# Optimization experiments

Hardware: AMD Instinct MI355X
Metric: run time of the kernel (lower is better)

## Reference

```python
import jax, jax.numpy as jnp
import numpy as np
import jax.lax as lax

H, D, C, CS, NS, OW, PD = 8, 64, 512, 64, 5, 8, 1
MAX_LR = 0.1
KCONV = 4


def short_conv(x, w, b):
    # x: (B,T,Din) -> causal depthwise conv over time
    B, T, Din = x.shape
    xc = jnp.transpose(x, (0, 2, 1))
    xc = jnp.pad(xc, ((0, 0), (0, 0), (KCONV - 1, 0)))
    xc = lax.conv_general_dilated(xc, w, window_strides=(1,), padding='VALID',
                                  dimension_numbers=('NCW', 'OIW', 'NCW'),
                                  feature_group_count=Din)
    xc = xc + b[:, jnp.newaxis]
    return jnp.transpose(xc, (0, 2, 1))


def linear_scan(h_init, gates, inputs):
    # h_t = gate_t * h_{t-1} + input_t ; gates: (B,cs,H), inputs: (B,cs,H,...)
    extra = inputs.ndim - gates.ndim
    g = gates.reshape(gates.shape + (1,) * extra)
    first = g[:, 0:1] * h_init[:, jnp.newaxis] + inputs[:, 0:1]
    mod_in = jnp.concatenate([first, inputs[:, 1:]], axis=1)
    mod_g = jnp.concatenate([jnp.zeros_like(g[:, 0:1]), g[:, 1:]], axis=1)

    def assoc(a, bb):
        ga, xa = a
        gb, xb = bb
        return (ga * gb, gb * xa + xb)

    _, h_all = lax.associative_scan(assoc, (mod_g, mod_in), axis=1)
    return h_all, h_all[:, -1]


def omega_aggregate(u, gamma, w):
    cs = u.shape[1]
    cum = jnp.cumsum(gamma * u, axis=1)
    if w >= cs:
        return cum
    shifted = jnp.concatenate([jnp.zeros_like(cum[:, :w]), cum[:, :-w]], axis=1)
    return cum - shifted


def polar_express(S, steps):
    # Newton-Schulz quintic orthogonalization (Muon/Polar-Express coefficients)
    a, b, c = 3.4445, -4.7750, 2.0315
    n = jnp.sqrt(jnp.sum(S * S, axis=(-2, -1), keepdims=True))
    X = S / (n * 1.01 + 1e-7)
    for _ in range(steps):
        A = X @ jnp.swapaxes(X, -2, -1)
        X = a * X + (b * A + c * (A @ A)) @ X
    return X


def rms_norm(x):
    ms = jnp.mean(x * x, axis=-1, keepdims=True)
    return x * lax.rsqrt(ms + 1e-6)


def atlas_forward(x, Wq, Wk, Wv, Wproj, conv_q_w, conv_q_b, conv_k_w, conv_k_b,
                  conv_v_w, conv_v_b, ga_w, ga_b, ge_w, ge_b, gt_w, gt_b,
                  gg_w, gg_b, poly_coeffs, ln_gamma, W1_init, rg_w):
    B, T, _ = x.shape
    q = short_conv(x @ Wq.T, conv_q_w, conv_q_b).reshape(B, T, H, D)
    k = short_conv(x @ Wk.T, conv_k_w, conv_k_b).reshape(B, T, H, D)
    v = short_conv(x @ Wv.T, conv_v_w, conv_v_b).reshape(B, T, H, D)

    def phi(z):
        r = poly_coeffs[0] * z
        zp = z
        for i in range(1, PD):
            zp = zp * z
            r = r + poly_coeffs[i] * zp
        return r

    q, k = phi(q), phi(k)

    alpha = jax.nn.sigmoid(x @ ga_w.T + ga_b)          # (B,T,H) memory retention
    eta = MAX_LR * jax.nn.sigmoid(x @ ge_w.T + ge_b)   # learning rate
    theta = jax.nn.sigmoid(x @ gt_w.T + gt_b)          # momentum decay
    gamma = jax.nn.sigmoid(x @ gg_w.T + gg_b)          # omega context gate

    nC = T // CS

    def chunk(z):
        return jnp.moveaxis(z.reshape(B, nC, CS, *z.shape[2:]), 1, 0)

    q_ch, k_ch, v_ch = chunk(q), chunk(k), chunk(v)
    a_ch = chunk(alpha)[..., None]
    e_ch = chunk(eta)[..., None]
    t_ch = chunk(theta)[..., None]
    g_ch = chunk(gamma)[..., None]

    M0 = jnp.broadcast_to(W1_init, (B, H, D, D))
    S0 = jnp.zeros((B, H, D, D), x.dtype)

    def step(carry, inp):
        M, S = carry
        q_c, k_c, v_c, a_c, e_c, t_c, g_c = inp
        pred = jnp.einsum('bhvk,bchk->bchv', M, k_c)
        err = pred - v_c
        u = (2.0 / D) * jnp.einsum('bchv,bchk->bchvk', err, k_c)
        u = omega_aggregate(u, g_c[..., None], OW)
        mom_in = -(e_c[..., None] * u)
        chunk_S, S = linear_scan(S, jnp.squeeze(t_c, -1), mom_in)
        chunk_S_orth = polar_express(chunk_S, NS)
        M_all, M = linear_scan(M, jnp.squeeze(a_c, -1), chunk_S_orth)
        y_c = jnp.einsum('bchvk,bchk->bchv', M_all, q_c)
        return (M, S), y_c

    (_, _), y = lax.scan(step, (M0, S0), (q_ch, k_ch, v_ch, a_ch, e_ch, t_ch, g_ch))
    y = jnp.moveaxis(y, 0, 1).reshape(B, T, H, D)
    y = rms_norm(y) * (1.0 + ln_gamma)
    rg = jax.nn.sigmoid(x @ rg_w.T)          # (B,T,H) retrieve gate
    y = y * rg[..., None]
    return y.reshape(B, T, H * D) @ Wproj.T


def setup_inputs() -> dict:
    key = jax.random.key(0)
    ks = jax.random.split(key, 24)
    B, T = 2, 1024
    Din = H * D

    def lin(k, o, i):
        return jax.random.normal(k, (o, i), jnp.float32) * (1.0 / np.sqrt(i))

    bound = float(np.sqrt(6.0 / (D + D)))
    return dict(
        x=jax.random.normal(ks[0], (B, T, C), jnp.float32),
        Wq=lin(ks[1], Din, C), Wk=lin(ks[2], Din, C), Wv=lin(ks[3], Din, C),
        Wproj=lin(ks[4], C, Din),
        conv_q_w=jax.random.normal(ks[5], (Din, 1, KCONV), jnp.float32) * 0.02,
        conv_q_b=jnp.zeros(Din, jnp.float32),
        conv_k_w=jax.random.normal(ks[6], (Din, 1, KCONV), jnp.float32) * 0.02,
        conv_k_b=jnp.zeros(Din, jnp.float32),
        conv_v_w=jax.random.normal(ks[7], (Din, 1, KCONV), jnp.float32) * 0.02,
        conv_v_b=jnp.zeros(Din, jnp.float32),
        ga_w=lin(ks[8], H, C), ga_b=jnp.zeros(H, jnp.float32),
        ge_w=lin(ks[9], H, C), ge_b=jnp.zeros(H, jnp.float32),
        gt_w=lin(ks[10], H, C), gt_b=jnp.zeros(H, jnp.float32),
        gg_w=lin(ks[11], H, C), gg_b=jnp.zeros(H, jnp.float32),
        poly_coeffs=jnp.ones(PD, jnp.float32),
        ln_gamma=jnp.zeros((H, D), jnp.float32),
        W1_init=jax.random.uniform(ks[12], (H, D, D), jnp.float32, -bound, bound),
        rg_w=lin(ks[13], H, C),
    )


def reference(x, Wq, Wk, Wv, Wproj, conv_q_w, conv_q_b, conv_k_w, conv_k_b,
              conv_v_w, conv_v_b, ga_w, ga_b, ge_w, ge_b, gt_w, gt_b,
              gg_w, gg_b, poly_coeffs, ln_gamma, W1_init, rg_w):
    return atlas_forward(x, Wq, Wk, Wv, Wproj, conv_q_w, conv_q_b, conv_k_w,
                         conv_k_b, conv_v_w, conv_v_b, ga_w, ga_b, ge_w, ge_b,
                         gt_w, gt_b, gg_w, gg_b, poly_coeffs, ln_gamma,
                         W1_init, rg_w)
```

## Files before the change

kernel.cpp:

```cpp
#include <hip/hip_runtime.h>

#define B_ 2
#define T_ 1024
#define H_ 8
#define D_ 64
#define SW(r, c) ((c) ^ (((r) & 7) << 3))

typedef __attribute__((ext_vector_type(8))) short s8v;
typedef __attribute__((ext_vector_type(4))) short s4v;
typedef __attribute__((ext_vector_type(4))) float f4v;

__device__ __forceinline__ short f2bf(float f) {
  unsigned u = __float_as_uint(f);
  u += 0x7fffu + ((u >> 16) & 1u);
  return (short)(u >> 16);
}
__device__ __forceinline__ float bf2f(short s) {
  return __uint_as_float(((unsigned)(unsigned short)s) << 16);
}
__device__ __forceinline__ float sigm(float v) { return 1.0f / (1.0f + __expf(-v)); }

#define MFMA(a, b, c) __builtin_amdgcn_mfma_f32_16x16x32_bf16((a), (b), (c), 0, 0, 0)

__global__ __launch_bounds__(256) void gemm_bt(const float* __restrict__ A,
// ... 73 lines not shown
}

__global__ __launch_bounds__(256) void gemm_qkv(const float* __restrict__ A,
    const float* __restrict__ Wq, const float* __restrict__ Wk,
    const float* __restrict__ Wv,
    float* __restrict__ xq, float* __restrict__ xk, float* __restrict__ xv) {
  __shared__ short Ash[64][40], Asl[64][40];
  __shared__ short Bsh[64][40], Bsl[64][40];
  const int sel = blockIdx.y >> 3;
  const float* Bw = sel == 0 ? Wq : (sel == 1 ? Wk : Wv);
  float* Co = sel == 0 ? xq : (sel == 1 ? xk : xv);
  const int tid = threadIdx.x;
  const int lane = tid & 63;
  const int wv = tid >> 6;
  const int wr = (wv >> 1) * 32;
  const int wc = (wv & 1) * 32;
  const int m0 = blockIdx.x * 64;
  const int n0 = (blockIdx.y & 7) * 64;
  const int ldr = tid >> 2;
  const int ldc = (tid & 3) * 8;
  const int l15 = lane & 15;
  const int kq = (lane >> 4) * 8;
  f4v acc[2][2];
#pragma unroll
  for (int i = 0; i < 2; ++i)
#pragma unroll
    for (int j = 0; j < 2; ++j)
#pragma unroll
      for (int r = 0; r < 4; ++r) acc[i][j][r] = 0.0f;
  const float* ap = A + (size_t)(m0 + ldr) * 512 + ldc;
  const float* bp = Bw + (size_t)(n0 + ldr) * 512 + ldc;
#pragma unroll 1
  for (int kt = 0; kt < 512; kt += 32) {
    float4 av0 = *(const float4*)(ap + kt);
    float4 av1 = *(const float4*)(ap + kt + 4);
    float4 bv0 = *(const float4*)(bp + kt);
    float4 bv1 = *(const float4*)(bp + kt + 4);
    float af[8] = {av0.x, av0.y, av0.z, av0.w, av1.x, av1.y, av1.z, av1.w};
    float bf[8] = {bv0.x, bv0.y, bv0.z, bv0.w, bv1.x, bv1.y, bv1.z, bv1.w};
    s8v ah, al, bh, bl;
#pragma unroll
    for (int i = 0; i < 8; ++i) {
      short h = f2bf(af[i]); ah[i] = h; al[i] = f2bf(af[i] - bf2f(h));
      h = f2bf(bf[i]); bh[i] = h; bl[i] = f2bf(bf[i] - bf2f(h));
    }
    __syncthreads();
    *(s8v*)&Ash[ldr][ldc] = ah; *(s8v*)&Asl[ldr][ldc] = al;
    *(s8v*)&Bsh[ldr][ldc] = bh; *(s8v*)&Bsl[ldr][ldc] = bl;
    __syncthreads();
    s8v a0h = *(const s8v*)&Ash[wr + l15][kq];
    s8v a1h = *(const s8v*)&Ash[wr + 16 + l15][kq];
    s8v b0h = *(const s8v*)&Bsh[wc + l15][kq];
    s8v b1h = *(const s8v*)&Bsh[wc + 16 + l15][kq];
    s8v a0l = *(const s8v*)&Asl[wr + l15][kq];
    s8v a1l = *(const s8v*)&Asl[wr + 16 + l15][kq];
    s8v b0l = *(const s8v*)&Bsl[wc + l15][kq];
    s8v b1l = *(const s8v*)&Bsl[wc + 16 + l15][kq];
    acc[0][0] = MFMA(a0h, b0h, acc[0][0]);
    acc[0][1] = MFMA(a0h, b1h, acc[0][1]);
    acc[1][0] = MFMA(a1h, b0h, acc[1][0]);
    acc[1][1] = MFMA(a1h, b1h, acc[1][1]);
    acc[0][0] = MFMA(a0h, b0l, acc[0][0]);
    acc[0][1] = MFMA(a0h, b1l, acc[0][1]);
    acc[1][0] = MFMA(a1h, b0l, acc[1][0]);
    acc[1][1] = MFMA(a1h, b1l, acc[1][1]);
    acc[0][0] = MFMA(a0l, b0h, acc[0][0]);
    acc[0][1] = MFMA(a0l, b1h, acc[0][1]);
    acc[1][0] = MFMA(a1l, b0h, acc[1][0]);
    acc[1][1] = MFMA(a1l, b1h, acc[1][1]);
  }
#pragma unroll
  for (int m2 = 0; m2 < 2; ++m2)
#pragma unroll
    for (int n2 = 0; n2 < 2; ++n2)
#pragma unroll
      for (int r = 0; r < 4; ++r) {
        int row = m0 + wr + m2 * 16 + (lane >> 4) * 4 + r;
        int col = n0 + wc + n2 * 16 + l15;
        Co[(size_t)row * 512 + col] = acc[m2][n2][r];
      }
}

__global__ __launch_bounds__(256) void conv3_k(
    const float* __restrict__ xq, const float* __restrict__ xk,
    const float* __restrict__ xv,
    const float* __restrict__ cqw, const float* __restrict__ cqb,
    const float* __restrict__ ckw, const float* __restrict__ ckb,
    const float* __restrict__ cvw, const float* __restrict__ cvb,
    const float* __restrict__ pc,
    float* __restrict__ qb, float* __restrict__ kb, float* __restrict__ vb) {
  const int s = blockIdx.x >> 12;
  const int idx = ((blockIdx.x & 4095) << 8) + threadIdx.x;
  const float* in = s == 0 ? xq : (s == 1 ? xk : xv);
  const float* w  = s == 0 ? cqw : (s == 1 ? ckw : cvw);
  const float* bs = s == 0 ? cqb : (s == 1 ? ckb : cvb);
  float* o        = s == 0 ? qb : (s == 1 ? kb : vb);
  const int d = idx & 511;
  const int bt = idx >> 9;
  const int t = bt & (T_ - 1);
  float acc = bs[d];
#pragma unroll
  for (int j = 0; j < 4; ++j) {
    int tt = t - 3 + j;
    if (tt >= 0) acc += w[d * 4 + j] * in[(size_t)(bt - 3 + j) * 512 + d];
  }
  float sc = (s < 2) ? pc[0] : 1.0f;
  o[idx] = sc * acc;
}

__global__ __launch_bounds__(256) void gates_k(const float* __restrict__ x,
    const float* __restrict__ gaw, const float* __restrict__ gab,
    const float* __restrict__ gew, const float* __restrict__ geb,
    const float* __restrict__ gtw, const float* __restrict__ gtb,
    const float* __restrict__ ggw, const float* __restrict__ ggb,
    const float* __restrict__ rgw,
    float* __restrict__ alpha, float* __restrict__ eta,
    float* __restrict__ theta, float* __restrict__ gam, float* __restrict__ rg) {
  int wv = threadIdx.x >> 6, lane = threadIdx.x & 63;
  int bt = blockIdx.x * 4 + wv;
  float xr[8];
#pragma unroll
  for (int i = 0; i < 8; ++i) xr[i] = x[(size_t)bt * 512 + i * 64 + lane];
  for (int h = 0; h < 8; ++h) {
    float s0 = 0, s1 = 0, s2 = 0, s3 = 0, s4 = 0;
#pragma unroll
    for (int i = 0; i < 8; ++i) {
      float xv = xr[i];
      int o = h * 512 + i * 64 + lane;
      s0 += xv * gaw[o];
      s1 += xv * gew[o];
      s2 += xv * gtw[o];
      s3 += xv * ggw[o];
      s4 += xv * rgw[o];
    }
#pragma unroll
    for (int off = 32; off >= 1; off >>= 1) {
      s0 += __shfl_xor(s0, off);
      s1 += __shfl_xor(s1, off);
      s2 += __shfl_xor(s2, off);
      s3 += __shfl_xor(s3, off);
      s4 += __shfl_xor(s4, off);
    }
    if (lane == 0) {
      size_t o = (size_t)bt * 8 + h;
      alpha[o] = sigm(s0 + gab[h]);
      eta[o]   = 0.1f * sigm(s1 + geb[h]);
      theta[o] = sigm(s2 + gtb[h]);
      gam[o]   = sigm(s3 + ggb[h]);
      rg[o]    = sigm(s4);
    }
  }
}

__global__ __launch_bounds__(256) void init_carry(const float* __restrict__ w1,
    float* __restrict__ Mc, float* __restrict__ Sc) {
  int idx = blockIdx.x * 256 + threadIdx.x;
  Mc[idx] = w1[idx & 32767];
  Sc[idx] = 0.0f;
}

__global__ __launch_bounds__(256) void chunk_a(
    const float* __restrict__ kb, const float* __restrict__ vb,
    const float* __restrict__ eta, const float* __restrict__ theta,
    const float* __restrict__ gam,
    const float* __restrict__ Mc, float* __restrict__ Sc,
    float* __restrict__ chS, int ci) {
  __shared__ float KT[64][65];
  __shared__ float errl[4][68];
  __shared__ float Ml[4][64];
  __shared__ float ge_[64], gt_[64], gg_[64];
  const int tid = threadIdx.x;
  const int bh = blockIdx.x >> 4;
  const int vs = blockIdx.x & 15;
  const int b = bh >> 3, h = bh & 7;
  const int v0 = vs * 4;
  const int t0 = ci * 64;
  const int lane = tid & 63, q4 = tid >> 6;
  for (int it = 0; it < 16; ++it) {
    int c = it * 4 + q4;
    KT[lane][c] = kb[((size_t)(b * T_ + t0 + c) * H_ + h) * 64 + lane];
  }
  if (tid < 64) {
    size_t gi = (size_t)(b * T_ + t0 + tid) * H_ + h;
    ge_[tid] = eta[gi]; gt_[tid] = theta[gi]; gg_[tid] = gam[gi];
  }
  Ml[q4][lane] = Mc[((size_t)bh * 64 + v0 + q4) * 64 + lane];
  __syncthreads();
  {
    int c = lane, vr = q4;
    float p = 0.0f;
#pragma unroll
    for (int k2 = 0; k2 < 64; ++k2) p += KT[k2][c] * Ml[vr][k2];
    float vv = vb[((size_t)(b * T_ + t0 + c) * H_ + h) * 64 + v0 + vr];
    errl[vr][c] = p - vv;
  }
  __syncthreads();
  {
    const int kk = lane, vr = q4, v = v0 + vr;
    float S = Sc[((size_t)bh * 64 + v) * 64 + kk];
    float ring[8];
    float cum = 0.0f;
    float* out = chS + ((size_t)(b << 6) * 8 + h) * 4096 + (size_t)v * 64 + kk;
    for (int c8 = 0; c8 < 8; ++c8) {
#pragma unroll
      for (int j = 0; j < 8; ++j) {
        int c = c8 * 8 + j;
        float u = 0.03125f * errl[vr][c] * KT[kk][c];
        float gu = gg_[c] * u;
        cum += gu;
        if (c8 > 0) cum -= ring[j];
        ring[j] = gu;
        float mom = -ge_[c] * cum;
        S = gt_[c] * S + mom;
        out[(size_t)c * 32768] = S;
      }
    }
    Sc[((size_t)bh * 64 + v) * 64 + kk] = S;
  }
}

__device__ __forceinline__ void mm4(const short (*Ah)[64], const short (*Al)[64],
    const short (*Bh)[64], const short (*Bl)[64],
    int wr, int wc, int l15, int kq, int sp, f4v acc[2][2]) {
#pragma unroll
  for (int kt = 0; kt < 64; kt += 32) {
    const int ra0 = wr + l15, ra1 = wr + 16 + l15;
    const int rb0 = wc + l15, rb1 = wc + 16 + l15;
    s8v a0h = *(const s8v*)&Ah[ra0][SW(ra0, kt + kq)];
    s8v a1h = *(const s8v*)&Ah[ra1][SW(ra1, kt + kq)];
    s8v b0h = *(const s8v*)&Bh[rb0][SW(rb0, kt + kq)];
    s8v b1h = *(const s8v*)&Bh[rb1][SW(rb1, kt + kq)];
    acc[0][0] = MFMA(a0h, b0h, acc[0][0]);
    acc[0][1] = MFMA(a0h, b1h, acc[0][1]);
    acc[1][0] = MFMA(a1h, b0h, acc[1][0]);
    acc[1][1] = MFMA(a1h, b1h, acc[1][1]);
    if (sp) {
      s8v a0l = *(const s8v*)&Al[ra0][SW(ra0, kt + kq)];
      s8v a1l = *(const s8v*)&Al[ra1][SW(ra1, kt + kq)];
      s8v b0l = *(const s8v*)&Bl[rb0][SW(rb0, kt + kq)];
      s8v b1l = *(const s8v*)&Bl[rb1][SW(rb1, kt + kq)];
      acc[0][0] = MFMA(a0h, b0l, acc[0][0]);
      acc[0][1] = MFMA(a0h, b1l, acc[0][1]);
      acc[1][0] = MFMA(a1h, b0l, acc[1][0]);
      acc[1][1] = MFMA(a1h, b1l, acc[1][1]);
      acc[0][0] = MFMA(a0l, b0h, acc[0][0]);
      acc[0][1] = MFMA(a0l, b1h, acc[0][1]);
      acc[1][0] = MFMA(a1l, b0h, acc[1][0]);
      acc[1][1] = MFMA(a1l, b1h, acc[1][1]);
    }
  }
}

__global__ __launch_bounds__(256, 3) void polar_k(float* __restrict__ cs) {
  __shared__ short Xh[64][64], Xl[64][64];
  __shared__ short XTh[64][64], XTl[64][64];
  __shared__ short Zh[64][64], Zl[64][64];
  __shared__ float red[4];
  const int tid = threadIdx.x;
  const int lane = tid & 63;
  const int w = tid >> 6;
  const int wr = (w >> 1) * 32;
  const int wc = (w & 1) * 32;
  const int l15 = lane & 15;
  const int q4 = lane >> 4;
  const int kq = q4 * 8;
  float* base = cs + (size_t)blockIdx.x * 4096;
  float xr[2][2][4];
  float ss = 0.0f;
#pragma unroll
  for (int m2 = 0; m2 < 2; ++m2)
#pragma unroll
    for (int n2 = 0; n2 < 2; ++n2)
#pragma unroll
      for (int r = 0; r < 4; ++r) {
        float v = base[(wr + m2 * 16 + q4 * 4 + r) * 64 + wc + n2 * 16 + l15];
        xr[m2][n2][r] = v;
        ss += v * v;
      }
#pragma unroll
  for (int off = 32; off >= 1; off >>= 1) ss += __shfl_xor(ss, off);
  if (lane == 0) red[w] = ss;
  __syncthreads();
  float scale = 1.0f / (sqrtf(red[0] + red[1] + red[2] + red[3]) * 1.01f + 1e-7f);
#pragma unroll
  for (int m2 = 0; m2 < 2; ++m2)
#pragma unroll
    for (int n2 = 0; n2 < 2; ++n2) {
      const int rr0 = wr + m2 * 16 + q4 * 4;
      const int cc = wc + n2 * 16 + l15;
      s4v hv, lv;
#pragma unroll
      for (int r = 0; r < 4; ++r) {
        float xv = xr[m2][n2][r] * scale;
        xr[m2][n2][r] = xv;
        short hh = f2bf(xv);
        short ll = f2bf(xv - bf2f(hh));
        hv[r] = hh; lv[r] = ll;
        Xh[rr0 + r][SW(rr0 + r, cc)] = hh;
        Xl[rr0 + r][SW(rr0 + r, cc)] = ll;
      }
      *(s4v*)&XTh[cc][SW(cc, rr0)] = hv;
      *(s4v*)&XTl[cc][SW(cc, rr0)] = lv;
    }
  __syncthreads();

#pragma unroll 1
  for (int it = 0; it < 5; ++it) {
    const int sp = (it < 4);
    f4v at[2][2];
#pragma unroll
    for (int m2 = 0; m2 < 2; ++m2)
#pragma unroll
      for (int n2 = 0; n2 < 2; ++n2)
#pragma unroll
        for (int r = 0; r < 4; ++r) at[m2][n2][r] = 0.0f;
    mm4(XTh, XTl, XTh, XTl, wr, wc, l15, kq, sp, at);
#pragma unroll
    for (int m2 = 0; m2 < 2; ++m2)
#pragma unroll
      for (int n2 = 0; n2 < 2; ++n2) {
        const int rr0 = wr + m2 * 16 + q4 * 4;
        const int cc = wc + n2 * 16 + l15;
        s4v hv, lv;
#pragma unroll
        for (int r = 0; r < 4; ++r) {
          float a = at[m2][n2][r];
          short hh = f2bf(a);
          hv[r] = hh; lv[r] = f2bf(a - bf2f(hh));
        }
        *(s4v*)&Zh[cc][SW(cc, rr0)] = hv;
        if (sp) *(s4v*)&Zl[cc][SW(cc, rr0)] = lv;
      }
    __syncthreads();
    f4v a2[2][2];
#pragma unroll
    for (int m2 = 0; m2 < 2; ++m2)
#pragma unroll
      for (int n2 = 0; n2 < 2; ++n2)
#pragma unroll
        for (int r = 0; r < 4; ++r) a2[m2][n2][r] = 0.0f;
    mm4(Zh, Zl, Zh, Zl, wr, wc, l15, kq, sp, a2);
    float zt[2][2][4];
#pragma unroll
    for (int m2 = 0; m2 < 2; ++m2)
#pragma unroll
      for (int n2 = 0; n2 < 2; ++n2)
#pragma unroll
        for (int r = 0; r < 4; ++r)
          zt[m2][n2][r] = -4.7750f * at[m2][n2][r] + 2.0315f * a2[m2][n2][r];
    __syncthreads();
#pragma unroll
    for (int m2 = 0; m2 < 2; ++m2)
#pragma unroll
      for (int n2 = 0; n2 < 2; ++n2) {
        const int rr0 = wr + m2 * 16 + q4 * 4;
        const int cc = wc + n2 * 16 + l15;
        s4v hv, lv;
#pragma unroll
        for (int r = 0; r < 4; ++r) {
          float zv = zt[m2][n2][r];
          short hh = f2bf(zv);
          hv[r] = hh; lv[r] = f2bf(zv - bf2f(hh));
        }
        *(s4v*)&Zh[cc][SW(cc, rr0)] = hv;
        if (sp) *(s4v*)&Zl[cc][SW(cc, rr0)] = lv;
      }
    __syncthreads();
    f4v q3[2][2];
#pragma unroll
    for (int m2 = 0; m2 < 2; ++m2)
#pragma unroll
      for (int n2 = 0; n2 < 2; ++n2)
#pragma unroll
        for (int r = 0; r < 4; ++r) q3[m2][n2][r] = 0.0f;
    mm4(Xh, Xl, Zh, Zl, wr, wc, l15, kq, sp, q3);
#pragma unroll
    for (int m2 = 0; m2 < 2; ++m2)
#pragma unroll
      for (int n2 = 0; n2 < 2; ++n2)
#pragma unroll
        for (int r = 0; r < 4; ++r)
          xr[m2][n2][r] = 3.4445f * xr[m2][n2][r] + q3[m2][n2][r];
    if (it < 4) {
      __syncthreads();
      const int slo = (it < 3);
#pragma unroll
      for (int m2 = 0; m2 < 2; ++m2)
#pragma unroll
        for (int n2 = 0; n2 < 2; ++n2) {
          const int rr0 = wr + m2 * 16 + q4 * 4;
          const int cc = wc + n2 * 16 + l15;
          s4v hv, lv;
#pragma unroll
          for (int r = 0; r < 4; ++r) {
            float xv = xr[m2][n2][r];
            short hh = f2bf(xv);
            short ll = f2bf(xv - bf2f(hh));
            hv[r] = hh; lv[r] = ll;
            Xh[rr0 + r][SW(rr0 + r, cc)] = hh;
            if (slo) Xl[rr0 + r][SW(rr0 + r, cc)] = ll;
          }
          *(s4v*)&XTh[cc][SW(cc, rr0)] = hv;
          if (slo) *(s4v*)&XTl[cc][SW(cc, rr0)] = lv;
        }
      __syncthreads();
    }
  }
#pragma unroll
  for (int m2 = 0; m2 < 2; ++m2)
#pragma unroll
    for (int n2 = 0; n2 < 2; ++n2)
#pragma unroll
      for (int r = 0; r < 4; ++r)
        base[(wr + m2 * 16 + q4 * 4 + r) * 64 + wc + n2 * 16 + l15] = xr[m2][n2][r];
}

__global__ __launch_bounds__(256, 1) void chunk_ca(
    const float* __restrict__ qb, const float* __restrict__ kb,
    const float* __restrict__ vb,
    const float* __restrict__ alpha, const float* __restrict__ eta,
    const float* __restrict__ theta, const float* __restrict__ gam,
    float* __restrict__ Mc, float* __restrict__ Sc,
    float* __restrict__ chS, float* __restrict__ yb, int ci) {
  __shared__ float KT[64][65];
  __shared__ float errl[4][68];
  __shared__ float Ml[4][64];
  __shared__ float ge_[64], gt_[64], gg_[64];
  const int tid = threadIdx.x, lane = tid & 63, w = tid >> 6;
  const int bh = blockIdx.x >> 4, vs = blockIdx.x & 15;
  const int b = bh >> 3, h = bh & 7;
  const int v0 = vs * 4, v = v0 + w;
  const int t0 = ci * 64;
  float M = Mc[((size_t)bh * 64 + v) * 64 + lane];
  const float* op = chS + ((size_t)(b << 6) * 8 + h) * 4096 + (size_t)v * 64 + lane;
  const float* qp = qb + ((size_t)(b * T_ + t0) * 8 + h) * 64 + lane;
  float* yp = yb + ((size_t)(b * T_ + t0) * 8 + h) * 64 + v;
  float av = alpha[(size_t)(b * T_ + t0 + lane) * 8 + h];
#pragma unroll
  for (int half = 0; half < 2; ++half) {
    const int cb = half * 32;
    float ov[32], qv[32], p[32];
#pragma unroll
    for (int j = 0; j < 32; ++j) ov[j] = op[(size_t)(cb + j) * 32768];
#pragma unroll
    for (int j = 0; j < 32; ++j) qv[j] = qp[(size_t)(cb + j) * 512];
#pragma unroll
    for (int j = 0; j < 32; ++j) {
      M = __builtin_fmaf(__shfl(av, cb + j), M, ov[j]);
      p[j] = M * qv[j];
    }
#pragma unroll
    for (int j = 0; j < 32; ++j) {
#pragma unroll
      for (int off = 32; off >= 1; off >>= 1) p[j] += __shfl_xor(p[j], off);
    }
    if (lane == 0) {
#pragma unroll
      for (int j = 0; j < 32; ++j) yp[(size_t)(cb + j) * 512] = p[j];
    }
  }
  Mc[((size_t)bh * 64 + v) * 64 + lane] = M;
  if (ci == 15) return;
  const int t1 = t0 + 64;
  Ml[w][lane] = M;
  for (int it = 0; it < 16; ++it) {
    int c = it * 4 + w;
    KT[lane][c] = kb[((size_t)(b * T_ + t1 + c) * 8 + h) * 64 + lane];
  }
  if (tid < 64) {
    size_t gi = (size_t)(b * T_ + t1 + tid) * 8 + h;
    ge_[tid] = eta[gi]; gt_[tid] = theta[gi]; gg_[tid] = gam[gi];
  }
  __syncthreads();
  {
    int c = lane, vr = w;
    float s0 = 0, s1 = 0, s2 = 0, s3 = 0;
#pragma unroll
    for (int k2 = 0; k2 < 64; k2 += 4) {
      s0 += KT[k2 + 0][c] * Ml[vr][k2 + 0];
      s1 += KT[k2 + 1][c] * Ml[vr][k2 + 1];
      s2 += KT[k2 + 2][c] * Ml[vr][k2 + 2];
      s3 += KT[k2 + 3][c] * Ml[vr][k2 + 3];
    }
    float vv = vb[((size_t)(b * T_ + t1 + c) * 8 + h) * 64 + v0 + vr];
    errl[vr][c] = (s0 + s1) + (s2 + s3) - vv;
  }
  __syncthreads();
  {
    const int kk = lane, vr = w, vv2 = v0 + vr;
    float S = Sc[((size_t)bh * 64 + vv2) * 64 + kk];
    float ring[8];
    float cum = 0.0f;
    float* out = chS + ((size_t)(b << 6) * 8 + h) * 4096 + (size_t)vv2 * 64 + kk;
    for (int c8 = 0; c8 < 8; ++c8) {
#pragma unroll
      for (int j = 0; j < 8; ++j) {
        int c = c8 * 8 + j;
        float u = 0.03125f * errl[vr][c] * KT[kk][c];
        float gu = gg_[c] * u;
        cum += gu;
        if (c8 > 0) cum -= ring[j];
        ring[j] = gu;
        float mom = -ge_[c] * cum;
        S = gt_[c] * S + mom;
        out[(size_t)c * 32768] = S;
      }
    }
    Sc[((size_t)bh * 64 + vv2) * 64 + kk] = S;
  }
}

__global__ __launch_bounds__(256) void norm_k(const float* __restrict__ yb,
    const float* __restrict__ lng, const float* __restrict__ rg,
    float* __restrict__ yn) {
  const int lane = threadIdx.x & 63;
  const int gw = blockIdx.x * 4 + (threadIdx.x >> 6);
  const int h = gw & 7;
  const int bt = gw >> 3;
  float y = yb[(size_t)gw * 64 + lane];
  float s = y * y;
#pragma unroll
  for (int off = 32; off >= 1; off >>= 1) s += __shfl_xor(s, off);
  float r = rsqrtf(s * (1.0f / 64.0f) + 1e-6f);
  yn[(size_t)gw * 64 + lane] = y * r * (1.0f + lng[h * 64 + lane]) * rg[(size_t)bt * 8 + h];
}

extern "C" void kernel_launch(void* const* d_in, const int* in_sizes, int n_in,
                              void* d_out, int out_size, void* d_ws, size_t ws_size,
                              hipStream_t stream) {
  (void)in_sizes; (void)n_in; (void)out_size; (void)ws_size;
  const float* x   = (const float*)d_in[0];
  const float* Wq  = (const float*)d_in[1];
  const float* Wk  = (const float*)d_in[2];
  const float* Wv  = (const float*)d_in[3];
  const float* Wpr = (const float*)d_in[4];
  const float* cqw = (const float*)d_in[5];
  const float* cqb = (const float*)d_in[6];
  const float* ckw = (const float*)d_in[7];
  const float* ckb = (const float*)d_in[8];
  const float* cvw = (const float*)d_in[9];
  const float* cvb = (const float*)d_in[10];
  const float* gaw = (const float*)d_in[11];
  const float* gab = (const float*)d_in[12];
  const float* gew = (const float*)d_in[13];
  const float* geb = (const float*)d_in[14];
  const float* gtw = (const float*)d_in[15];
  const float* gtb = (const float*)d_in[16];
  const float* ggw = (const float*)d_in[17];
  const float* ggb = (const float*)d_in[18];
  const float* pc  = (const float*)d_in[19];
  const float* lng = (const float*)d_in[20];
  const float* w1  = (const float*)d_in[21];
  const float* rgw = (const float*)d_in[22];
  float* outp = (float*)d_out;

  float* chS = (float*)d_ws;
  float* xq = chS;
  float* xk = chS + 1048576;
  float* xv = chS + 2 * 1048576;
  float* yn = chS;
  char* wp = (char*)d_ws + (size_t)16 * 1024 * 1024;
  auto alloc = [&](size_t bytes) {
    char* p = wp;
    wp += (bytes + 255) & ~(size_t)255;
    return p;
  };
  const size_t BT = (size_t)B_ * T_;
  float* qb = (float*)alloc(BT * 512 * 4);
  float* kb = (float*)alloc(BT * 512 * 4);
  float* vb = (float*)alloc(BT * 512 * 4);
  float* yb = (float*)alloc(BT * 512 * 4);
  float* alpha = (float*)alloc(BT * 8 * 4);
  float* eta   = (float*)alloc(BT * 8 * 4);
  float* theta = (float*)alloc(BT * 8 * 4);
  float* gam   = (float*)alloc(BT * 8 * 4);
  float* rg    = (float*)alloc(BT * 8 * 4);
  float* Mc = (float*)alloc((size_t)65536 * 4);
  float* Sc = (float*)alloc((size_t)65536 * 4);

  init_carry<<<dim3(256), dim3(256), 0, stream>>>(w1, Mc, Sc);
  gemm_qkv<<<dim3(32, 24), dim3(256), 0, stream>>>(x, Wq, Wk, Wv, xq, xk, xv);
  conv3_k<<<dim3(12288), dim3(256), 0, stream>>>(xq, xk, xv, cqw, cqb, ckw, ckb,
                                                 cvw, cvb, pc, qb, kb, vb);
  gates_k<<<dim3(512), dim3(256), 0, stream>>>(x, gaw, gab, gew, geb, gtw, gtb,
                                               ggw, ggb, rgw, alpha, eta, theta, gam, rg);
  chunk_a<<<dim3(256), dim3(256), 0, stream>>>(kb, vb, eta, theta, gam, Mc, Sc, chS, 0);
  for (int ci = 0; ci < 16; ++ci) {
    polar_k<<<dim3(1024), dim3(256), 0, stream>>>(chS);
    chunk_ca<<<dim3(256), dim3(256), 0, stream>>>(qb, kb, vb, alpha, eta, theta, gam,
                                                  Mc, Sc, chS, yb, ci);
  }
  norm_k<<<dim3(4096), dim3(256), 0, stream>>>(yb, lng, rg, yn);
  gemm_bt<<<dim3(32, 8), dim3(256), 0, stream>>>(yn, Wpr, outp, 2048, 512, 512);
}
```

Baseline: 1.048 ms.

## Fuse chunk recurrence and polar iterations into one persistent kernel with flag barriers

Replaces the 33 per-chunk launches of chunk_a/polar_k/chunk_ca with a single persistent kernel of 512 blocks. The blocks for each batch-head pair synchronise through global atomic counters instead of kernel boundaries, and the M/S carries stay in registers instead of going through global memory. Warps 2-3 prefetch the next chunk's keys and gates while warps 0-1 run the output phase. This removes launch and drain overhead, at the cost of spin-wait barriers that require all 512 blocks to be co-resident, plus lower parallelism per phase.

```diff
diff --git a/kernel.cpp b/kernel.cpp
--- a/kernel.cpp
+++ b/kernel.cpp
@@ -249,169 +249,178 @@
   }
 }
 
-__global__ __launch_bounds__(256) void init_carry(const float* __restrict__ w1,
-    float* __restrict__ Mc, float* __restrict__ Sc) {
-  int idx = blockIdx.x * 256 + threadIdx.x;
-  Mc[idx] = w1[idx & 32767];
-  Sc[idx] = 0.0f;
-}
-
-__global__ __launch_bounds__(256) void chunk_a(
-    const float* __restrict__ kb, const float* __restrict__ vb,
+__global__ __launch_bounds__(256, 2) void atlas_persist(
+    const float* __restrict__ qb, const float* __restrict__ kb,
+    const float* __restrict__ vb, const float* __restrict__ alpha,
     const float* __restrict__ eta, const float* __restrict__ theta,
-    const float* __restrict__ gam,
-    const float* __restrict__ Mc, float* __restrict__ Sc,
-    float* __restrict__ chS, int ci) {
-  __shared__ float KT[64][65];
-  __shared__ float errl[4][68];
-  __shared__ float Ml[4][64];
-  __shared__ float ge_[64], gt_[64], gg_[64];
-  const int tid = threadIdx.x;
-  const int bh = blockIdx.x >> 4;
-  const int vs = blockIdx.x & 15;
-  const int b = bh >> 3, h = bh & 7;
-  const int v0 = vs * 4;
-  const int t0 = ci * 64;
-  const int lane = tid & 63, q4 = tid >> 6;
-  for (int it = 0; it < 16; ++it) {
-    int c = it * 4 + q4;
-    KT[lane][c] = kb[((size_t)(b * T_ + t0 + c) * H_ + h) * 64 + lane];
-  }
-  if (tid < 64) {
-    size_t gi = (size_t)(b * T_ + t0 + tid) * H_ + h;
-    ge_[tid] = eta[gi]; gt_[tid] = theta[gi]; gg_[tid] = gam[gi];
-  }
-  Ml[q4][lane] = Mc[((size_t)bh * 64 + v0 + q4) * 64 + lane];
-  __syncthreads();
-  {
-    int c = lane, vr = q4;
-    float p = 0.0f;
-#pragma unroll
-    for (int k2 = 0; k2 < 64; ++k2) p += KT[k2][c] * Ml[vr][k2];
-    float vv = vb[((size_t)(b * T_ + t0 + c) * H_ + h) * 64 + v0 + vr];
-    errl[vr][c] = p - vv;
-  }
-  __syncthreads();
-  {
-    const int kk = lane, vr = q4, v = v0 + vr;
-    float S = Sc[((size_t)bh * 64 + v) * 64 + kk];
-    float ring[8];
-    float cum = 0.0f;
-    float* out = chS + ((size_t)(b << 6) * 8 + h) * 4096 + (size_t)v * 64 + kk;
-    for (int c8 = 0; c8 < 8; ++c8) {
-#pragma unroll
-      for (int j = 0; j < 8; ++j) {
-        int c = c8 * 8 + j;
-        float u = 0.03125f * errl[vr][c] * KT[kk][c];
-        float gu = gg_[c] * u;
-        cum += gu;
-        if (c8 > 0) cum -= ring[j];
-        ring[j] = gu;
-        float mom = -ge_[c] * cum;
-        S = gt_[c] * S + mom;
-        out[(size_t)c * 32768] = S;
-      }
-    }
-    Sc[((size_t)bh * 64 + v) * 64 + kk] = S;
-  }
-}
-
-__device__ __forceinline__ void mm4(const short (*Ah)[64], const short (*Al)[64],
-    const short (*Bh)[64], const short (*Bl)[64],
-    int wr, int wc, int l15, int kq, int sp, f4v acc[2][2]) {
-#pragma unroll
-  for (int kt = 0; kt < 64; kt += 32) {
-    const int ra0 = wr + l15, ra1 = wr + 16 + l15;
-    const int rb0 = wc + l15, rb1 = wc + 16 + l15;
-    s8v a0h = *(const s8v*)&Ah[ra0][SW(ra0, kt + kq)];
-    s8v a1h = *(const s8v*)&Ah[ra1][SW(ra1, kt + kq)];
-    s8v b0h = *(const s8v*)&Bh[rb0][SW(rb0, kt + kq)];
-    s8v b1h = *(const s8v*)&Bh[rb1][SW(rb1, kt + kq)];
-    acc[0][0] = MFMA(a0h, b0h, acc[0][0]);
-    acc[0][1] = MFMA(a0h, b1h, acc[0][1]);
-    acc[1][0] = MFMA(a1h, b0h, acc[1][0]);
-    acc[1][1] = MFMA(a1h, b1h, acc[1][1]);
-    if (sp) {
-      s8v a0l = *(const s8v*)&Al[ra0][SW(ra0, kt + kq)];
-      s8v a1l = *(const s8v*)&Al[ra1][SW(ra1, kt + kq)];
-      s8v b0l = *(const s8v*)&Bl[rb0][SW(rb0, kt + kq)];
-      s8v b1l = *(const s8v*)&Bl[rb1][SW(rb1, kt + kq)];
-      acc[0][0] = MFMA(a0h, b0l, acc[0][0]);
-      acc[0][1] = MFMA(a0h, b1l, acc[0][1]);
-      acc[1][0] = MFMA(a1h, b0l, acc[1][0]);
-      acc[1][1] = MFMA(a1h, b1l, acc[1][1]);
-      acc[0][0] = MFMA(a0l, b0h, acc[0][0]);
-      acc[0][1] = MFMA(a0l, b1h, acc[0][1]);
-      acc[1][0] = MFMA(a1l, b0h, acc[1][0]);
-      acc[1][1] = MFMA(a1l, b1h, acc[1][1]);
-    }
-  }
-}
-
-__global__ __launch_bounds__(256, 3) void polar_k(float* __restrict__ cs) {
+    const float* __restrict__ gam, const float* __restrict__ w1,
+    float* __restrict__ chS, float* __restrict__ yb,
+    unsigned* __restrict__ flags) {
   __shared__ short Xh[64][64], Xl[64][64];
   __shared__ short XTh[64][64], XTl[64][64];
   __shared__ short Zh[64][64], Zl[64][64];
   __shared__ float red[4];
+  __shared__ float KT[64][65];
+  __shared__ float Ml[2][64], errl[2][64];
+  __shared__ float ge_[64], gt_[64], gg_[64];
+
   const int tid = threadIdx.x;
   const int lane = tid & 63;
   const int w = tid >> 6;
-  const int wr = (w >> 1) * 32;
-  const int wc = (w & 1) * 32;
-  const int l15 = lane & 15;
-  const int q4 = lane >> 4;
-  const int kq = q4 * 8;
-  float* base = cs + (size_t)blockIdx.x * 4096;
-  float xr[2][2][4];
-  float ss = 0.0f;
-#pragma unroll
-  for (int m2 = 0; m2 < 2; ++m2)
-#pragma unroll
-    for (int n2 = 0; n2 < 2; ++n2)
-#pragma unroll
-      for (int r = 0; r < 4; ++r) {
-        float v = base[(wr + m2 * 16 + q4 * 4 + r) * 64 + wc + n2 * 16 + l15];
-        xr[m2][n2][r] = v;
-        ss += v * v;
-      }
-#pragma unroll
-  for (int off = 32; off >= 1; off >>= 1) ss += __shfl_xor(ss, off);
-  if (lane == 0) red[w] = ss;
-  __syncthreads();
-  float scale = 1.0f / (sqrtf(red[0] + red[1] + red[2] + red[3]) * 1.01f + 1e-7f);
-#pragma unroll
-  for (int m2 = 0; m2 < 2; ++m2)
-#pragma unroll
-    for (int n2 = 0; n2 < 2; ++n2) {
-      const int rr0 = wr + m2 * 16 + q4 * 4;
-      const int cc = wc + n2 * 16 + l15;
-      s4v hv, lv;
-#pragma unroll
-      for (int r = 0; r < 4; ++r) {
-        float xv = xr[m2][n2][r] * scale;
-        xr[m2][n2][r] = xv;
-        short hh = f2bf(xv);
-        short ll = f2bf(xv - bf2f(hh));
-        hv[r] = hh; lv[r] = ll;
-        Xh[rr0 + r][SW(rr0 + r, cc)] = hh;
-        Xl[rr0 + r][SW(rr0 + r, cc)] = ll;
-      }
-      *(s4v*)&XTh[cc][SW(cc, rr0)] = hv;
-      *(s4v*)&XTl[cc][SW(cc, rr0)] = lv;
-    }
-  __syncthreads();
-
-#pragma unroll 1
-  for (int it = 0; it < 5; ++it) {
-    const int sp = (it < 4);
-    f4v at[2][2];
+  const int g = blockIdx.x;
+  const int bh = g & 15, sub = g >> 4;
+  const int b = bh >> 3, h = bh & 7;
+  unsigned* flag = flags + bh * 32;
+  const int wr = (w >> 1) * 32, wc = (w & 1) * 32;
+  const int l15 = lane & 15, q4 = lane >> 4, kq = q4 * 8;
+  const size_t matbase = ((size_t)(b << 6) * 8 + h) * 4096;
+  const int v = 2 * sub + w;
+
+  float M = 0.0f, S = 0.0f;
+
+  auto ARRIVE = [&]() {
+    __threadfence();
+    __syncthreads();
+    if (tid == 0)
+      __hip_atomic_fetch_add(flag, 1u, __ATOMIC_RELEASE, __HIP_MEMORY_SCOPE_AGENT);
+  };
+  auto WAIT = [&](int n) {
+    if (tid == 0) {
+      unsigned tgt = 32u * (unsigned)n;
+      while (__hip_atomic_load(flag, __ATOMIC_ACQUIRE, __HIP_MEMORY_SCOPE_AGENT) < tgt)
+        __builtin_amdgcn_s_sleep(2);
+      __threadfence();
+    }
+    __syncthreads();
+  };
+  auto LOADKT = [&](int cb) {
+    const int t = cb * 64;
+    const int tl = tid - 128;
+    for (int i = tl; i < 4096; i += 128) {
+      int k = i & 63, c = i >> 6;
+      KT[k][c] = kb[((size_t)(b * T_ + t + c) * 8 + h) * 64 + k];
+    }
+    if (tl < 64) {
+      size_t gi = (size_t)(b * T_ + t + tl) * 8 + h;
+      ge_[tl] = eta[gi]; gt_[tl] = theta[gi]; gg_[tl] = gam[gi];
+    }
+  };
+  auto PHASEB = [&](int cb) {
+    const int t = cb * 64;
+    Ml[w][lane] = M;
+    {
+      int c = lane;
+      float s0 = 0, s1 = 0, s2 = 0, s3 = 0;
+#pragma unroll
+      for (int k2 = 0; k2 < 64; k2 += 4) {
+        s0 += KT[k2 + 0][c] * Ml[w][k2 + 0];
+        s1 += KT[k2 + 1][c] * Ml[w][k2 + 1];
+        s2 += KT[k2 + 2][c] * Ml[w][k2 + 2];
+        s3 += KT[k2 + 3][c] * Ml[w][k2 + 3];
+      }
+      float vv = vb[((size_t)(b * T_ + t + c) * 8 + h) * 64 + v];
+      errl[w][c] = (s0 + s1) + (s2 + s3) - vv;
+    }
+    {
+      float ring[8];
+      float cum = 0.0f;
+      float* out = chS + matbase + (size_t)v * 64 + lane;
+      for (int c8 = 0; c8 < 8; ++c8) {
+#pragma unroll
+        for (int j = 0; j < 8; ++j) {
+          int c = c8 * 8 + j;
+          float u = 0.03125f * errl[w][c] * KT[lane][c];
+          float gu = gg_[c] * u;
+          cum += gu;
+          if (c8 > 0) cum -= ring[j];
+          ring[j] = gu;
+          float mom = -ge_[c] * cum;
+          S = gt_[c] * S + mom;
+          out[(size_t)c * 32768] = S;
+        }
+      }
+    }
+  };
+  auto PHASEA = [&](int ci) {
+    const int t0 = ci * 64;
+    const float* op = chS + matbase + (size_t)v * 64 + lane;
+    const float* qp = qb + ((size_t)(b * T_ + t0) * 8 + h) * 64 + lane;
+    float* yp = yb + ((size_t)(b * T_ + t0) * 8 + h) * 64 + v;
+    float av = alpha[(size_t)(b * T_ + t0 + lane) * 8 + h];
+#pragma unroll
+    for (int half = 0; half < 2; ++half) {
+      const int cb2 = half * 32;
+      float ov[32], qv[32], p[32];
+#pragma unroll
+      for (int j = 0; j < 32; ++j) ov[j] = op[(size_t)(cb2 + j) * 32768];
+#pragma unroll
+      for (int j = 0; j < 32; ++j) qv[j] = qp[(size_t)(cb2 + j) * 512];
+#pragma unroll
+      for (int j = 0; j < 32; ++j) {
+        M = __builtin_fmaf(__shfl(av, cb2 + j), M, ov[j]);
+        p[j] = M * qv[j];
+      }
+#pragma unroll
+      for (int j = 0; j < 32; ++j) {
+#pragma unroll
+        for (int off = 32; off >= 1; off >>= 1) p[j] += __shfl_xor(p[j], off);
+      }
+      if (lane == 0) {
+#pragma unroll
+        for (int j = 0; j < 32; ++j) yp[(size_t)(cb2 + j) * 512] = p[j];
+      }
+    }
+  };
+  auto MM4 = [&](const short (*Ah)[64], const short (*Al)[64],
+                 const short (*Bh)[64], const short (*Bl)[64],
+                 int sp, f4v acc[2][2]) {
+#pragma unroll
+    for (int kt = 0; kt < 64; kt += 32) {
+      const int ra0 = wr + l15, ra1 = wr + 16 + l15;
+      const int rb0 = wc + l15, rb1 = wc + 16 + l15;
+      s8v a0h = *(const s8v*)&Ah[ra0][SW(ra0, kt + kq)];
+      s8v a1h = *(const s8v*)&Ah[ra1][SW(ra1, kt + kq)];
+      s8v b0h = *(const s8v*)&Bh[rb0][SW(rb0, kt + kq)];
+      s8v b1h = *(const s8v*)&Bh[rb1][SW(rb1, kt + kq)];
+      acc[0][0] = MFMA(a0h, b0h, acc[0][0]);
+      acc[0][1] = MFMA(a0h, b1h, acc[0][1]);
+      acc[1][0] = MFMA(a1h, b0h, acc[1][0]);
+      acc[1][1] = MFMA(a1h, b1h, acc[1][1]);
+      if (sp) {
+        s8v a0l = *(const s8v*)&Al[ra0][SW(ra0, kt + kq)];
+        s8v a1l = *(const s8v*)&Al[ra1][SW(ra1, kt + kq)];
+        s8v b0l = *(const s8v*)&Bl[rb0][SW(rb0, kt + kq)];
+        s8v b1l = *(const s8v*)&Bl[rb1][SW(rb1, kt + kq)];
+        acc[0][0] = MFMA(a0h, b0l, acc[0][0]);
+        acc[0][1] = MFMA(a0h, b1l, acc[0][1]);
+        acc[1][0] = MFMA(a1h, b0l, acc[1][0]);
+        acc[1][1] = MFMA(a1h, b1l, acc[1][1]);
+        acc[0][0] = MFMA(a0l, b0h, acc[0][0]);
+        acc[0][1] = MFMA(a0l, b1h, acc[0][1]);
+        acc[1][0] = MFMA(a1l, b0h, acc[1][0]);
+        acc[1][1] = MFMA(a1l, b1h, acc[1][1]);
+      }
+    }
+  };
+  auto POLAR = [&](int c) {
+    float* base = chS + ((size_t)((b * 64 + c) * 8) + h) * 4096;
+    float xr[2][2][4];
+    float ss = 0.0f;
 #pragma unroll
     for (int m2 = 0; m2 < 2; ++m2)
 #pragma unroll
       for (int n2 = 0; n2 < 2; ++n2)
 #pragma unroll
-        for (int r = 0; r < 4; ++r) at[m2][n2][r] = 0.0f;
-    mm4(XTh, XTl, XTh, XTl, wr, wc, l15, kq, sp, at);
+        for (int r = 0; r < 4; ++r) {
+          float vv = base[(wr + m2 * 16 + q4 * 4 + r) * 64 + wc + n2 * 16 + l15];
+          xr[m2][n2][r] = vv;
+          ss += vv * vv;
+        }
+#pragma unroll
+    for (int off = 32; off >= 1; off >>= 1) ss += __shfl_xor(ss, off);
+    if (lane == 0) red[w] = ss;
+    __syncthreads();
+    float scale = 1.0f / (sqrtf(red[0] + red[1] + red[2] + red[3]) * 1.01f + 1e-7f);
 #pragma unroll
     for (int m2 = 0; m2 < 2; ++m2)
 #pragma unroll
@@ -421,66 +430,29 @@
         s4v hv, lv;
 #pragma unroll
         for (int r = 0; r < 4; ++r) {
-          float a = at[m2][n2][r];
-          short hh = f2bf(a);
-          hv[r] = hh; lv[r] = f2bf(a - bf2f(hh));
+          float xv = xr[m2][n2][r] * scale;
+          xr[m2][n2][r] = xv;
+          short hh = f2bf(xv);
+          short ll = f2bf(xv - bf2f(hh));
+          hv[r] = hh; lv[r] = ll;
+          Xh[rr0 + r][SW(rr0 + r, cc)] = hh;
+          Xl[rr0 + r][SW(rr0 + r, cc)] = ll;
         }
-        *(s4v*)&Zh[cc][SW(cc, rr0)] = hv;
-        if (sp) *(s4v*)&Zl[cc][SW(cc, rr0)] = lv;
-      }
-    __syncthreads();
-    f4v a2[2][2];
-#pragma unroll
-    for (int m2 = 0; m2 < 2; ++m2)
-#pragma unroll
-      for (int n2 = 0; n2 < 2; ++n2)
-#pragma unroll
-        for (int r = 0; r < 4; ++r) a2[m2][n2][r] = 0.0f;
-    mm4(Zh, Zl, Zh, Zl, wr, wc, l15, kq, sp, a2);
-    float zt[2][2][4];
-#pragma unroll
-    for (int m2 = 0; m2 < 2; ++m2)
-#pragma unroll
-      for (int n2 = 0; n2 < 2; ++n2)
-#pragma unroll
-        for (int r = 0; r < 4; ++r)
-          zt[m2][n2][r] = -4.7750f * at[m2][n2][r] + 2.0315f * a2[m2][n2][r];
-    __syncthreads();
-#pragma unroll
-    for (int m2 = 0; m2 < 2; ++m2)
-#pragma unroll
-      for (int n2 = 0; n2 < 2; ++n2) {
-        const int rr0 = wr + m2 * 16 + q4 * 4;
-        const int cc = wc + n2 * 16 + l15;
-        s4v hv, lv;
-#pragma unroll
-        for (int r = 0; r < 4; ++r) {
-          float zv = zt[m2][n2][r];
-          short hh = f2bf(zv);
-          hv[r] = hh; lv[r] = f2bf(zv - bf2f(hh));
-        }
-        *(s4v*)&Zh[cc][SW(cc, rr0)] = hv;
-        if (sp) *(s4v*)&Zl[cc][SW(cc, rr0)] = lv;
-      }
-    __syncthreads();
-    f4v q3[2][2];
-#pragma unroll
-    for (int m2 = 0; m2 < 2; ++m2)
-#pragma unroll
-      for (int n2 = 0; n2 < 2; ++n2)
-#pragma unroll
-        for (int r = 0; r < 4; ++r) q3[m2][n2][r] = 0.0f;
-    mm4(Xh, Xl, Zh, Zl, wr, wc, l15, kq, sp, q3);
-#pragma unroll
-    for (int m2 = 0; m2 < 2; ++m2)
-#pragma unroll
-      for (int n2 = 0; n2 < 2; ++n2)
-#pragma unroll
-        for (int r = 0; r < 4; ++r)
-          xr[m2][n2][r] = 3.4445f * xr[m2][n2][r] + q3[m2][n2][r];
-    if (it < 4) {
-      __syncthreads();
-      const int slo = (it < 3);
+        *(s4v*)&XTh[cc][SW(cc, rr0)] = hv;
+        *(s4v*)&XTl[cc][SW(cc, rr0)] = lv;
+      }
+    __syncthreads();
+#pragma unroll 1
+    for (int it = 0; it < 5; ++it) {
+      const int sp = (it < 4);
+      f4v at[2][2];
+#pragma unroll
+      for (int m2 = 0; m2 < 2; ++m2)
+#pragma unroll
+        for (int n2 = 0; n2 < 2; ++n2)
+#pragma unroll
+          for (int r = 0; r < 4; ++r) at[m2][n2][r] = 0.0f;
+      MM4(XTh, XTl, XTh, XTl, sp, at);
 #pragma unroll
       for (int m2 = 0; m2 < 2; ++m2)
 #pragma unroll
@@ -490,120 +462,122 @@
           s4v hv, lv;
 #pragma unroll
           for (int r = 0; r < 4; ++r) {
-            float xv = xr[m2][n2][r];
-            short hh = f2bf(xv);
-            short ll = f2bf(xv - bf2f(hh));
-            hv[r] = hh; lv[r] = ll;
-            Xh[rr0 + r][SW(rr0 + r, cc)] = hh;
-            if (slo) Xl[rr0 + r][SW(rr0 + r, cc)] = ll;
+            float a = at[m2][n2][r];
+            short hh = f2bf(a);
+            hv[r] = hh; lv[r] = f2bf(a - bf2f(hh));
           }
-          *(s4v*)&XTh[cc][SW(cc, rr0)] = hv;
-          if (slo) *(s4v*)&XTl[cc][SW(cc, rr0)] = lv;
+          *(s4v*)&Zh[cc][SW(cc, rr0)] = hv;
+          if (sp) *(s4v*)&Zl[cc][SW(cc, rr0)] = lv;
         }
       __syncthreads();
-    }
-  }
-#pragma unroll
-  for (int m2 = 0; m2 < 2; ++m2)
-#pragma unroll
-    for (int n2 = 0; n2 < 2; ++n2)
-#pragma unroll
-      for (int r = 0; r < 4; ++r)
-        base[(wr + m2 * 16 + q4 * 4 + r) * 64 + wc + n2 * 16 + l15] = xr[m2][n2][r];
-}
-
-__global__ __launch_bounds__(256, 1) void chunk_ca(
-    const float* __restrict__ qb, const float* __restrict__ kb,
-    const float* __restrict__ vb,
-    const float* __restrict__ alpha, const float* __restrict__ eta,
-    const float* __restrict__ theta, const float* __restrict__ gam,
-    float* __restrict__ Mc, float* __restrict__ Sc,
-    float* __restrict__ chS, float* __restrict__ yb, int ci) {
-  __shared__ float KT[64][65];
-  __shared__ float errl[4][68];
-  __shared__ float Ml[4][64];
-  __shared__ float ge_[64], gt_[64], gg_[64];
-  const int tid = threadIdx.x, lane = tid & 63, w = tid >> 6;
-  const int bh = blockIdx.x >> 4, vs = blockIdx.x & 15;
-  const int b = bh >> 3, h = bh & 7;
-  const int v0 = vs * 4, v = v0 + w;
-  const int t0 = ci * 64;
-  float M = Mc[((size_t)bh * 64 + v) * 64 + lane];
-  const float* op = chS + ((size_t)(b << 6) * 8 + h) * 4096 + (size_t)v * 64 + lane;
-  const float* qp = qb + ((size_t)(b * T_ + t0) * 8 + h) * 64 + lane;
-  float* yp = yb + ((size_t)(b * T_ + t0) * 8 + h) * 64 + v;
-  float av = alpha[(size_t)(b * T_ + t0 + lane) * 8 + h];
-#pragma unroll
-  for (int half = 0; half < 2; ++half) {
-    const int cb = half * 32;
-    float ov[32], qv[32], p[32];
-#pragma unroll
-    for (int j = 0; j < 32; ++j) ov[j] = op[(size_t)(cb + j) * 32768];
-#pragma unroll
-    for (int j = 0; j < 32; ++j) qv[j] = qp[(size_t)(cb + j) * 512];
-#pragma unroll
-    for (int j = 0; j < 32; ++j) {
-      M = __builtin_fmaf(__shfl(av, cb + j), M, ov[j]);
-      p[j] = M * qv[j];
-    }
-#pragma unroll
-    for (int j = 0; j < 32; ++j) {
-#pragma unroll
-      for (int off = 32; off >= 1; off >>= 1) p[j] += __shfl_xor(p[j], off);
-    }
-    if (lane == 0) {
-#pragma unroll
-      for (int j = 0; j < 32; ++j) yp[(size_t)(cb + j) * 512] = p[j];
-    }
-  }
-  Mc[((size_t)bh * 64 + v) * 64 + lane] = M;
-  if (ci == 15) return;
-  const int t1 = t0 + 64;
-  Ml[w][lane] = M;
-  for (int it = 0; it < 16; ++it) {
-    int c = it * 4 + w;
-    KT[lane][c] = kb[((size_t)(b * T_ + t1 + c) * 8 + h) * 64 + lane];
-  }
-  if (tid < 64) {
-    size_t gi = (size_t)(b * T_ + t1 + tid) * 8 + h;
-    ge_[tid] = eta[gi]; gt_[tid] = theta[gi]; gg_[tid] = gam[gi];
+      f4v a2[2][2];
+#pragma unroll
+      for (int m2 = 0; m2 < 2; ++m2)
+#pragma unroll
+        for (int n2 = 0; n2 < 2; ++n2)
+#pragma unroll
+          for (int r = 0; r < 4; ++r) a2[m2][n2][r] = 0.0f;
+      MM4(Zh, Zl, Zh, Zl, sp, a2);
+      float zt[2][2][4];
+#pragma unroll
+      for (int m2 = 0; m2 < 2; ++m2)
+#pragma unroll
+        for (int n2 = 0; n2 < 2; ++n2)
+#pragma unroll
+          for (int r = 0; r < 4; ++r)
+            zt[m2][n2][r] = -4.7750f * at[m2][n2][r] + 2.0315f * a2[m2][n2][r];
+      __syncthreads();
+#pragma unroll
+      for (int m2 = 0; m2 < 2; ++m2)
+#pragma unroll
+        for (int n2 = 0; n2 < 2; ++n2) {
+          const int rr0 = wr + m2 * 16 + q4 * 4;
+          const int cc = wc + n2 * 16 + l15;
+          s4v hv, lv;
+#pragma unroll
+          for (int r = 0; r < 4; ++r) {
+            float zv = zt[m2][n2][r];
+            short hh = f2bf(zv);
+            hv[r] = hh; lv[r] = f2bf(zv - bf2f(hh));
+          }
+          *(s4v*)&Zh[cc][SW(cc, rr0)] = hv;
+          if (sp) *(s4v*)&Zl[cc][SW(cc, rr0)] = lv;
+        }
+      __syncthreads();
+      f4v q3[2][2];
+#pragma unroll
+      for (int m2 = 0; m2 < 2; ++m2)
+#pragma unroll
+        for (int n2 = 0; n2 < 2; ++n2)
+#pragma unroll
+          for (int r = 0; r < 4; ++r) q3[m2][n2][r] = 0.0f;
+      MM4(Xh, Xl, Zh, Zl, sp, q3);
+#pragma unroll
+      for (int m2 = 0; m2 < 2; ++m2)
+#pragma unroll
+        for (int n2 = 0; n2 < 2; ++n2)
+#pragma unroll
+          for (int r = 0; r < 4; ++r)
+            xr[m2][n2][r] = 3.4445f * xr[m2][n2][r] + q3[m2][n2][r];
+      if (it < 4) {
+        __syncthreads();
+        const int slo = (it < 3);
+#pragma unroll
+        for (int m2 = 0; m2 < 2; ++m2)
+#pragma unroll
+          for (int n2 = 0; n2 < 2; ++n2) {
+            const int rr0 = wr + m2 * 16 + q4 * 4;
+            const int cc = wc + n2 * 16 + l15;
+            s4v hv, lv;
+#pragma unroll
+            for (int r = 0; r < 4; ++r) {
+              float xv = xr[m2][n2][r];
+              short hh = f2bf(xv);
+              short ll = f2bf(xv - bf2f(hh));
+              hv[r] = hh; lv[r] = ll;
+              Xh[rr0 + r][SW(rr0 + r, cc)] = hh;
+              if (slo) Xl[rr0 + r][SW(rr0 + r, cc)] = ll;
+            }
+            *(s4v*)&XTh[cc][SW(cc, rr0)] = hv;
+            if (slo) *(s4v*)&XTl[cc][SW(cc, rr0)] = lv;
+          }
+        __syncthreads();
+      }
+    }
+#pragma unroll
+    for (int m2 = 0; m2 < 2; ++m2)
+#pragma unroll
+      for (int n2 = 0; n2 < 2; ++n2)
+#pragma unroll
+        for (int r = 0; r < 4; ++r)
+          base[(wr + m2 * 16 + q4 * 4 + r) * 64 + wc + n2 * 16 + l15] = xr[m2][n2][r];
+    __syncthreads();
+  };
+
+  if (w < 2) {
+    M = w1[(size_t)h * 4096 + (size_t)v * 64 + lane];
+    S = 0.0f;
+  } else {
+    LOADKT(0);
   }
   __syncthreads();
-  {
-    int c = lane, vr = w;
-    float s0 = 0, s1 = 0, s2 = 0, s3 = 0;
-#pragma unroll
-    for (int k2 = 0; k2 < 64; k2 += 4) {
-      s0 += KT[k2 + 0][c] * Ml[vr][k2 + 0];
-      s1 += KT[k2 + 1][c] * Ml[vr][k2 + 1];
-      s2 += KT[k2 + 2][c] * Ml[vr][k2 + 2];
-      s3 += KT[k2 + 3][c] * Ml[vr][k2 + 3];
-    }
-    float vv = vb[((size_t)(b * T_ + t1 + c) * 8 + h) * 64 + v0 + vr];
-    errl[vr][c] = (s0 + s1) + (s2 + s3) - vv;
-  }
-  __syncthreads();
-  {
-    const int kk = lane, vr = w, vv2 = v0 + vr;
-    float S = Sc[((size_t)bh * 64 + vv2) * 64 + kk];
-    float ring[8];
-    float cum = 0.0f;
-    float* out = chS + ((size_t)(b << 6) * 8 + h) * 4096 + (size_t)vv2 * 64 + kk;
-    for (int c8 = 0; c8 < 8; ++c8) {
-#pragma unroll
-      for (int j = 0; j < 8; ++j) {
-        int c = c8 * 8 + j;
-        float u = 0.03125f * errl[vr][c] * KT[kk][c];
-        float gu = gg_[c] * u;
-        cum += gu;
-        if (c8 > 0) cum -= ring[j];
-        ring[j] = gu;
-        float mom = -ge_[c] * cum;
-        S = gt_[c] * S + mom;
-        out[(size_t)c * 32768] = S;
-      }
-    }
-    Sc[((size_t)bh * 64 + vv2) * 64 + kk] = S;
+  if (w < 2) PHASEB(0);
+  ARRIVE();
+
+#pragma unroll 1
+  for (int ci = 0; ci < 16; ++ci) {
+    WAIT(2 * ci + 1);
+#pragma unroll 1
+    for (int m = 0; m < 2; ++m) POLAR(2 * sub + m);
+    ARRIVE();
+    WAIT(2 * ci + 2);
+    if (w < 2) PHASEA(ci);
+    else if (ci < 15) LOADKT(ci + 1);
+    __syncthreads();
+    if (ci < 15) {
+      if (w < 2) PHASEB(ci + 1);
+      ARRIVE();
+    }
   }
 }
 
@@ -672,21 +646,16 @@
   float* theta = (float*)alloc(BT * 8 * 4);
   float* gam   = (float*)alloc(BT * 8 * 4);
   float* rg    = (float*)alloc(BT * 8 * 4);
-  float* Mc = (float*)alloc((size_t)65536 * 4);
-  float* Sc = (float*)alloc((size_t)65536 * 4);
-
-  init_carry<<<dim3(256), dim3(256), 0, stream>>>(w1, Mc, Sc);
+  unsigned* flags = (unsigned*)alloc(16 * 32 * 4);
+
+  hipMemsetAsync(flags, 0, 16 * 32 * 4, stream);
   gemm_qkv<<<dim3(32, 24), dim3(256), 0, stream>>>(x, Wq, Wk, Wv, xq, xk, xv);
   conv3_k<<<dim3(12288), dim3(256), 0, stream>>>(xq, xk, xv, cqw, cqb, ckw, ckb,
                                                  cvw, cvb, pc, qb, kb, vb);
   gates_k<<<dim3(512), dim3(256), 0, stream>>>(x, gaw, gab, gew, geb, gtw, gtb,
                                                ggw, ggb, rgw, alpha, eta, theta, gam, rg);
-  chunk_a<<<dim3(256), dim3(256), 0, stream>>>(kb, vb, eta, theta, gam, Mc, Sc, chS, 0);
-  for (int ci = 0; ci < 16; ++ci) {
-    polar_k<<<dim3(1024), dim3(256), 0, stream>>>(chS);
-    chunk_ca<<<dim3(256), dim3(256), 0, stream>>>(qb, kb, vb, alpha, eta, theta, gam,
-                                                  Mc, Sc, chS, yb, ci);
-  }
+  atlas_persist<<<dim3(512), dim3(256), 0, stream>>>(qb, kb, vb, alpha, eta, theta,
+                                                     gam, w1, chS, yb, flags);
   norm_k<<<dim3(4096), dim3(256), 0, stream>>>(yb, lng, rg, yn);
   gemm_bt<<<dim3(32, 8), dim3(256), 0, stream>>>(yn, Wpr, outp, 2048, 512, 512);
 }
```

New measurement: 3.839 ms. +266.3%, slower.
